# Kernel optimization log

Measured on AMD Instinct MI355X. Metric: run time of the kernel, lower is better.

Reference implementation:

```python
import jax, jax.numpy as jnp
import numpy as np

B, S, D, H = 2, 2048, 1024, 16
DEPTH = D // H


def setup_inputs() -> dict:
    key = jax.random.key(0)
    ks = jax.random.split(key, 8)
    w_scale = 0.02
    # causal mask: 1.0 where attention is NOT allowed (added as mask * -1e9)
    causal = jnp.triu(jnp.ones((S, S), dtype=jnp.float32), k=1)[None, None]  # [1,1,S,S]
    return {
        "q": jax.random.normal(ks[0], (B, S, D), dtype=jnp.float32),
        "k": jax.random.normal(ks[1], (B, S, D), dtype=jnp.float32),
        "v": jax.random.normal(ks[2], (B, S, D), dtype=jnp.float32),
        "mask": causal,
        "Wq": jax.random.normal(ks[3], (D, D), dtype=jnp.float32) * w_scale,
        "bq": jnp.zeros((D,), dtype=jnp.float32),
        "Wk": jax.random.normal(ks[4], (D, D), dtype=jnp.float32) * w_scale,
        "bk": jnp.zeros((D,), dtype=jnp.float32),
        "Wv": jax.random.normal(ks[5], (D, D), dtype=jnp.float32) * w_scale,
        "bv": jnp.zeros((D,), dtype=jnp.float32),
        "Wo": jax.random.normal(ks[6], (D, D), dtype=jnp.float32) * w_scale,
        "bo": jnp.zeros((D,), dtype=jnp.float32),
    }


def _split_heads(x):
    # [B,S,D] -> [B,H,S,depth]
    return x.reshape(B, S, H, DEPTH).transpose(0, 2, 1, 3)


def reference(q, k, v, mask, Wq, bq, Wk, bk, Wv, bv, Wo, bo):
    qh = _split_heads(q @ Wq + bq)
    kh = _split_heads(k @ Wk + bk)
    vh = _split_heads(v @ Wv + bv)
    scale = 1.0 / jnp.sqrt(jnp.asarray(DEPTH, dtype=qh.dtype))
    logits = jnp.einsum('bhqd,bhkd->bhqk', qh, kh) * scale  # [B,H,S,S]
    logits = logits + mask * (-1e9)
    attn = jax.nn.softmax(logits, axis=-1)
    out = jnp.einsum('bhqk,bhkd->bhqd', attn, vh)  # [B,H,S,depth]
    out = out.transpose(0, 2, 1, 3).reshape(B, S, D)
    return out @ Wo + bo
```

## Files before the change

kernel.cpp:

```cpp
#include <hip/hip_runtime.h>


typedef unsigned short u16;
typedef unsigned int u32;

using bf16x8 = __attribute__((ext_vector_type(8))) short;
using bf16x4 = __attribute__((ext_vector_type(4))) short;
using f32x4  = __attribute__((ext_vector_type(4))) float;

#define SEQ 2048
#define DMODEL 1024
#define NHEAD 16
#define DEPTH 64
#define BATCH 2
#define M_ROWS (BATCH * SEQ)

__device__ __forceinline__ u16 f2bf(float f) {
    union { float f; u32 u; } v; v.f = f;
    u32 u = v.u;
    return (u16)((u + 0x7FFFu + ((u >> 16) & 1u)) >> 16);
}
__device__ __forceinline__ u16 f2bf_trunc(float f) {
    union { float f; u32 u; } v; v.f = f;
    return (u16)(v.u >> 16);
}

__device__ __forceinline__ float hw_exp2(float x) {
#if __has_builtin(__builtin_amdgcn_exp2f)
    return __builtin_amdgcn_exp2f(x);
#else
    float r;
    asm("v_exp_f32 %0, %1" : "=v"(r) : "v"(x));
    return r;
#endif
}

__device__ __forceinline__ f32x4 mfma16(bf16x8 a, bf16x8 b, f32x4 c) {
    return __builtin_amdgcn_mfma_f32_16x16x32_bf16(a, b, c, 0, 0, 0);
}

__device__ __forceinline__ void glds16(const u16* src, u16* dst) {
    __builtin_amdgcn_global_load_lds((const __attribute__((address_space(1))) void*)src,
                                     (__attribute__((address_space(3))) void*)dst,
                                     16, 0, 0);
}

__device__ __forceinline__ bf16x8 fragld(const u16* base, int lr, int gc) {
    return *(const bf16x8*)(base + lr * 64 + (((gc ^ lr) & 7) << 3));
}
__device__ __forceinline__ bf16x8 fragld32(const u16* base, int lr, int gc) {
    return *(const bf16x8*)(base + lr * 32 + (((gc ^ lr) & 3) << 3));
}

__global__ __launch_bounds__(256) void prep_kernel(
        const float* __restrict__ q, const float* __restrict__ k,
        const float* __restrict__ v,
        u16* __restrict__ qo, u16* __restrict__ ko, u16* __restrict__ vo,
        const float* __restrict__ Wq, const float* __restrict__ Wk,
        const float* __restrict__ Wv, const float* __restrict__ Wo,
        u16* __restrict__ Wqt, u16* __restrict__ Wkt,
        u16* __restrict__ Wvt, u16* __restrict__ Wot) {
    int bid = blockIdx.x;
    if (bid < 12288) {
        const float* in; u16* out;
        int z = bid >> 12, bx = bid & 4095;
        if (z == 0)      { in = q; out = qo; }
        else if (z == 1) { in = k; out = ko; }
        else             { in = v; out = vo; }
        int idx = bx * 256 + threadIdx.x;
        float4 val = ((const float4*)in)[idx];
        ushort4 o;
        o.x = f2bf(val.x); o.y = f2bf(val.y); o.z = f2bf(val.z); o.w = f2bf(val.w);
        ((ushort4*)out)[idx] = o;
    } else {
        __shared__ float tile[32][33];
        int wid = bid - 12288;
        int z = wid >> 10, rem = wid & 1023;
        const float* W; u16* Wt;
        switch (z) {
            case 0: W = Wq; Wt = Wqt; break;
            case 1: W = Wk; Wt = Wkt; break;
            case 2: W = Wv; Wt = Wvt; break;
            default: W = Wo; Wt = Wot; break;
        }
        int k0 = (rem & 31) * 32, n0 = (rem >> 5) * 32;
        int tx = threadIdx.x & 31, ty = threadIdx.x >> 5;
#pragma unroll
        for (int i = 0; i < 4; ++i)
            tile[ty + 8 * i][tx] = W[(size_t)(k0 + ty + 8 * i) * DMODEL + n0 + tx];
        __syncthreads();
#pragma unroll
        for (int i = 0; i < 4; ++i)
            Wt[(size_t)(n0 + ty + 8 * i) * DMODEL + k0 + tx] = f2bf(tile[tx][ty + 8 * i]);
    }
}

template<int TM>
__device__ __forceinline__ void gemm_core(const u16* __restrict__ A, const u16* __restrict__ Bt,
                                          const float* __restrict__ bias,
                                          u16* __restrict__ outb, float* __restrict__ outf,
                                          int mode, float oscale, int bm0, int bn0) {
    constexpr int K = DMODEL;
    constexpr int NT = K / 32;
    constexpr int MI = TM / 32;
    constexpr int ACH = TM / 64;
    __shared__ u16 As[2][TM * 32];
    __shared__ u16 Bs[2][128 * 32];
    int t = threadIdx.x;
    int w = t >> 6, lane = t & 63, l15 = lane & 15, quad = lane >> 4;
    int wm = (w >> 1) * (TM / 2), wn = (w & 1) * 64;
    int r16 = lane >> 2, g4 = lane & 3;
    int gswz = ((g4 ^ (r16 & 3)) << 3);
    f32x4 acc[MI][4] = {};

#define QSTAGE(p, kt) do { \
    _Pragma("unroll") for (int c = 0; c < ACH; ++c) { \
        int ch = w * ACH + c; \
        glds16(A + (size_t)(bm0 + ch * 16 + r16) * K + (kt) * 32 + gswz, &As[p][ch * 512]); } \
    _Pragma("unroll") for (int c = 0; c < 2; ++c) { \
        int ch = w * 2 + c; \
        glds16(Bt + (size_t)(bn0 + ch * 16 + r16) * K + (kt) * 32 + gswz, &Bs[p][ch * 512]); } \
    } while (0)

    QSTAGE(0, 0);
    __syncthreads();

    for (int kt = 0; kt < NT; ++kt) {
        int cur = kt & 1;
        if (kt + 1 < NT) QSTAGE(cur ^ 1, kt + 1);
        bf16x8 af[MI], bfr[4];
#pragma unroll
        for (int i = 0; i < MI; ++i) af[i]  = fragld32(&As[cur][0], wm + i * 16 + l15, quad);
#pragma unroll
        for (int j = 0; j < 4;  ++j) bfr[j] = fragld32(&Bs[cur][0], wn + j * 16 + l15, quad);
#pragma unroll
        for (int i = 0; i < MI; ++i)
#pragma unroll
            for (int j = 0; j < 4; ++j)
                acc[i][j] = mfma16(af[i], bfr[j], acc[i][j]);
        __syncthreads();
    }
#undef QSTAGE

#pragma unroll
    for (int i = 0; i < MI; ++i) {
        int row_g0 = bm0 + wm + i * 16 + quad * 4;
#pragma unroll
        for (int j = 0; j < 4; ++j) {
            int col_g = bn0 + wn + j * 16 + l15;
            float bsv = bias[col_g];
#pragma unroll
            for (int r = 0; r < 4; ++r) {
                float v = (acc[i][j][r] + bsv) * oscale;
                int rg = row_g0 + r;
                if (mode == 2) {
                    outf[(size_t)rg * DMODEL + col_g] = v;
                } else {
                    int b = rg >> 11, s = rg & (SEQ - 1);
                    int h = col_g >> 6, d = col_g & 63;
                    size_t idx;
                    if (mode == 0) idx = ((size_t)(b * NHEAD + h) * SEQ + s) * DEPTH + d;
                    else           idx = ((size_t)(b * NHEAD + h) * DEPTH + d) * SEQ + s;
                    outb[idx] = f2bf(v);
                }
            }
        }
    }
}

#define SCALE_Q 0.1803368801111204f

__global__ __launch_bounds__(256, 4) void gemm_qkv(
        const u16* __restrict__ qb, const u16* __restrict__ kb, const u16* __restrict__ vb,
        const u16* __restrict__ Wqt, const u16* __restrict__ Wkt, const u16* __restrict__ Wvt,
        const float* __restrict__ bq, const float* __restrict__ bk, const float* __restrict__ bv,
        u16* __restrict__ Qp, u16* __restrict__ Kp, u16* __restrict__ Vpt) {
    int id = blockIdx.x;
    int c = id & 7, m = id >> 3;
    int slab = c * 12 + (m >> 3);
    int x = m & 7;
    int z = slab >> 5, y = slab & 31;
    int bm0 = y * 128, bn0 = x * 128;
    if (z == 0)      gemm_core<128>(qb, Wqt, bq, Qp,  nullptr, 0, SCALE_Q, bm0, bn0);
    else if (z == 1) gemm_core<128>(kb, Wkt, bk, Kp,  nullptr, 0, 1.0f,    bm0, bn0);
    else             gemm_core<128>(vb, Wvt, bv, Vpt, nullptr, 1, 1.0f,    bm0, bn0);
}

__global__ __launch_bounds__(256, 4) void gemm_out(
        const u16* __restrict__ attnb, const u16* __restrict__ Wot,
        const float* __restrict__ bo, float* __restrict__ out) {
    int id = blockIdx.x;
    int c = id & 7, m = id >> 3;
    int slab = c * 8 + (m >> 3);
    int x = m & 7;
    gemm_core<64>(attnb, Wot, bo, nullptr, out, 2, 1.0f, slab * 64, x * 128);
}

#define LP 72
__global__ __launch_bounds__(256) void attn_kernel(
        const u16* __restrict__ Qp, const u16* __restrict__ Kp,
        const u16* __restrict__ Vpt, u16* __restrict__ attn_out) {
    __shared__ u16 Klds[2][64 * 64];
    __shared__ u16 Vtlds[3][64 * 64];
    __shared__ u16 Plds[4 * 16 * LP];
    int t = threadIdx.x, w = t >> 6, lane = t & 63, l15 = lane & 15, quad = lane >> 4;
    int r8 = lane >> 3, g8 = lane & 7;
    int gswz = ((g8 ^ r8) << 3);
    u16* Pw = Plds + w * 16 * LP;

    int id = blockIdx.x;
    int xcd = id & 7, li = id >> 3;
    int bh = xcd * 4 + (li & 3);
    int pi = li >> 2;
    int b = bh >> 4, h = bh & 15;
    const u16* Qbase = Qp  + (size_t)bh * SEQ * DEPTH;
    const u16* Kbase = Kp  + (size_t)bh * SEQ * DEPTH;
    const u16* Vbase = Vpt + (size_t)bh * DEPTH * SEQ;

    bf16x8 ones;
#pragma unroll
    for (int i = 0; i < 8; ++i) ones[i] = (short)0x3F80;

    for (int half = 0; half < 2; ++half) {
        int qt = half ? pi : (31 - pi);
        int q0 = qt * 64;
        int nkt = qt + 1;
        __syncthreads();

        int qrow = q0 + w * 16 + l15;
        bf16x8 qf[2];
        qf[0] = *(const bf16x8*)(Qbase + (size_t)qrow * DEPTH + quad * 8);
        qf[1] = *(const bf16x8*)(Qbase + (size_t)qrow * DEPTH + 32 + quad * 8);

        f32x4 of[4] = {};
        f32x4 lacc = {};
        bf16x8 pfp[2];

#pragma unroll
        for (int c2 = 0; c2 < 2; ++c2) {
            int ch = w * 2 + c2;
            glds16(Kbase + (size_t)(ch * 8 + r8) * DEPTH + gswz, Klds[0] + ch * 512);
            glds16(Vbase + (size_t)(ch * 8 + r8) * SEQ + gswz,   Vtlds[0] + ch * 512);
        }

        for (int kt = 0; kt < nkt; ++kt) {
            int kc = kt & 1;
            __syncthreads();
            if (kt + 1 < nkt) {
                int kn = kt + 1, knx = kn & 1, vnx = kn % 3;
#pragma unroll
                for (int c2 = 0; c2 < 2; ++c2) {
                    int ch = w * 2 + c2;
                    glds16(Kbase + (size_t)(kn * 64 + ch * 8 + r8) * DEPTH + gswz,
                           Klds[knx] + ch * 512);
                    glds16(Vbase + (size_t)(ch * 8 + r8) * SEQ + kn * 64 + gswz,
                           Vtlds[vnx] + ch * 512);
                }
            }
            f32x4 st[4] = {};
            __builtin_amdgcn_s_setprio(1);
#pragma unroll
            for (int nt = 0; nt < 4; ++nt)
#pragma unroll
                for (int kk = 0; kk < 2; ++kk)
                    st[nt] = mfma16(fragld(Klds[kc], nt * 16 + l15, kk * 4 + quad), qf[kk], st[nt]);
            __builtin_amdgcn_s_setprio(0);

            if (kt > 0) {
                int vp = (kt - 1) % 3;
                __builtin_amdgcn_s_setprio(1);
#pragma unroll
                for (int kk = 0; kk < 2; ++kk) {
                    lacc = mfma16(pfp[kk], ones, lacc);
#pragma unroll
                    for (int nt = 0; nt < 4; ++nt)
                        of[nt] = mfma16(pfp[kk], fragld(Vtlds[vp], nt * 16 + l15, kk * 4 + quad), of[nt]);
                }
                __builtin_amdgcn_s_setprio(0);
            }

            bool diag = (kt == nkt - 1);
            int qlv = w * 16 + l15;
#pragma unroll
            for (int nt = 0; nt < 4; ++nt) {
                bf16x4 pv;
#pragma unroll
                for (int r = 0; r < 4; ++r) {
                    float e = hw_exp2(st[nt][r]);
                    if (diag) {
                        int keyl = nt * 16 + quad * 4 + r;
                        e = (keyl > qlv) ? 0.f : e;
                    }
                    pv[r] = (short)f2bf_trunc(e);
                }
                *(bf16x4*)(Pw + l15 * LP + nt * 16 + quad * 4) = pv;
            }
            asm volatile("" ::: "memory");
            pfp[0] = *(const bf16x8*)(Pw + l15 * LP + quad * 8);
            pfp[1] = *(const bf16x8*)(Pw + l15 * LP + 32 + quad * 8);
        }
        {
            int vp = (nkt - 1) % 3;
            __builtin_amdgcn_s_setprio(1);
#pragma unroll
            for (int kk = 0; kk < 2; ++kk) {
                lacc = mfma16(pfp[kk], ones, lacc);
#pragma unroll
                for (int nt = 0; nt < 4; ++nt)
                    of[nt] = mfma16(pfp[kk], fragld(Vtlds[vp], nt * 16 + l15, kk * 4 + quad), of[nt]);
            }
            __builtin_amdgcn_s_setprio(0);
        }
#pragma unroll
        for (int r = 0; r < 4; ++r) {
            float inv = 1.0f / lacc[r];
            int s_ = q0 + w * 16 + quad * 4 + r;
#pragma unroll
            for (int nt = 0; nt < 4; ++nt) {
                int dcol = h * DEPTH + nt * 16 + l15;
                attn_out[((size_t)(b * SEQ + s_)) * DMODEL + dcol] = f2bf(of[nt][r] * inv);
            }
        }
    }
}

extern "C" void kernel_launch(void* const* d_in, const int* in_sizes, int n_in,
                              void* d_out, int out_size, void* d_ws, size_t ws_size,
                              hipStream_t stream) {
    const float* q  = (const float*)d_in[0];
    const float* k  = (const float*)d_in[1];
    const float* v  = (const float*)d_in[2];
    const float* Wq = (const float*)d_in[4];
    const float* bq = (const float*)d_in[5];
    const float* Wk = (const float*)d_in[6];
    const float* bk = (const float*)d_in[7];
    const float* Wv = (const float*)d_in[8];
    const float* bv = (const float*)d_in[9];
    const float* Wo = (const float*)d_in[10];
    const float* bo = (const float*)d_in[11];
    float* out = (float*)d_out;

    char* ws = (char*)d_ws;
    const size_t SZ_ACT = (size_t)M_ROWS * DMODEL * 2;
    const size_t SZ_W   = (size_t)DMODEL * DMODEL * 2;
    u16* qb   = (u16*)(ws);
    u16* kb   = (u16*)(ws + SZ_ACT);
    u16* vb   = (u16*)(ws + 2 * SZ_ACT);
    u16* Wqt  = (u16*)(ws + 3 * SZ_ACT);
    u16* Wkt  = (u16*)(ws + 3 * SZ_ACT + SZ_W);
    u16* Wvt  = (u16*)(ws + 3 * SZ_ACT + 2 * SZ_W);
    u16* Wot  = (u16*)(ws + 3 * SZ_ACT + 3 * SZ_W);
    u16* Qp   = (u16*)(ws + 3 * SZ_ACT + 4 * SZ_W);
    u16* Kp   = (u16*)(ws + 4 * SZ_ACT + 4 * SZ_W);
    u16* Vpt  = (u16*)(ws + 5 * SZ_ACT + 4 * SZ_W);
    u16* attnb= (u16*)(ws + 6 * SZ_ACT + 4 * SZ_W);

    prep_kernel<<<dim3(16384), 256, 0, stream>>>(q, k, v, qb, kb, vb,
                                                 Wq, Wk, Wv, Wo, Wqt, Wkt, Wvt, Wot);
    gemm_qkv<<<dim3(768), 256, 0, stream>>>(
        qb, kb, vb, Wqt, Wkt, Wvt, bq, bk, bv, Qp, Kp, Vpt);
    attn_kernel<<<dim3(512), 256, 0, stream>>>(Qp, Kp, Vpt, attnb);
    gemm_out<<<dim3(512), 256, 0, stream>>>(attnb, Wot, bo, out);
}
```

Baseline: 219.0 us.

## Process two KV tiles per barrier with four-deep K/V LDS ring

The attention inner loop now handles key tiles in pairs, prefetching the next two K/V tiles into a 4-slot LDS ring, and issues one __syncthreads per pair instead of per tile. Both QK^T products are computed before the two softmax/PV steps, which replaces the earlier skewed software pipeline in which PV of the previous tile overlapped the current QK. The aim is fewer barriers and more independent MFMA work per sync. In exchange it uses more LDS (Klds grows from 2 to 4 slots, Vtlds from 3 to 4), which may reduce occupancy, and it adds register pressure from two sets of score accumulators.

```diff
diff --git a/kernel.cpp b/kernel.cpp
--- a/kernel.cpp
+++ b/kernel.cpp
@@ -200,8 +200,8 @@
 __global__ __launch_bounds__(256) void attn_kernel(
         const u16* __restrict__ Qp, const u16* __restrict__ Kp,
         const u16* __restrict__ Vpt, u16* __restrict__ attn_out) {
-    __shared__ u16 Klds[2][64 * 64];
-    __shared__ u16 Vtlds[3][64 * 64];
+    __shared__ u16 Klds[4][64 * 64];
+    __shared__ u16 Vtlds[4][64 * 64];
     __shared__ u16 Plds[4 * 16 * LP];
     int t = threadIdx.x, w = t >> 6, lane = t & 63, l15 = lane & 15, quad = lane >> 4;
     int r8 = lane >> 3, g8 = lane & 7;
@@ -221,6 +221,16 @@
 #pragma unroll
     for (int i = 0; i < 8; ++i) ones[i] = (short)0x3F80;
 
+#define STAGE_KV(ktv) do { \
+    int _b3 = (ktv) & 3; \
+    _Pragma("unroll") for (int c2 = 0; c2 < 2; ++c2) { \
+        int ch = w * 2 + c2; \
+        glds16(Kbase + (size_t)((ktv) * 64 + ch * 8 + r8) * DEPTH + gswz, \
+               Klds[_b3] + ch * 512); \
+        glds16(Vbase + (size_t)(ch * 8 + r8) * SEQ + (ktv) * 64 + gswz, \
+               Vtlds[_b3] + ch * 512); } \
+    } while (0)
+
     for (int half = 0; half < 2; ++half) {
         int qt = half ? pi : (31 - pi);
         int q0 = qt * 64;
@@ -234,51 +244,11 @@
 
         f32x4 of[4] = {};
         f32x4 lacc = {};
-        bf16x8 pfp[2];
-
-#pragma unroll
-        for (int c2 = 0; c2 < 2; ++c2) {
-            int ch = w * 2 + c2;
-            glds16(Kbase + (size_t)(ch * 8 + r8) * DEPTH + gswz, Klds[0] + ch * 512);
-            glds16(Vbase + (size_t)(ch * 8 + r8) * SEQ + gswz,   Vtlds[0] + ch * 512);
-        }
-
-        for (int kt = 0; kt < nkt; ++kt) {
-            int kc = kt & 1;
-            __syncthreads();
-            if (kt + 1 < nkt) {
-                int kn = kt + 1, knx = kn & 1, vnx = kn % 3;
-#pragma unroll
-                for (int c2 = 0; c2 < 2; ++c2) {
-                    int ch = w * 2 + c2;
-                    glds16(Kbase + (size_t)(kn * 64 + ch * 8 + r8) * DEPTH + gswz,
-                           Klds[knx] + ch * 512);
-                    glds16(Vbase + (size_t)(ch * 8 + r8) * SEQ + kn * 64 + gswz,
-                           Vtlds[vnx] + ch * 512);
-                }
-            }
-            f32x4 st[4] = {};
-            __builtin_amdgcn_s_setprio(1);
-#pragma unroll
-            for (int nt = 0; nt < 4; ++nt)
-#pragma unroll
-                for (int kk = 0; kk < 2; ++kk)
-                    st[nt] = mfma16(fragld(Klds[kc], nt * 16 + l15, kk * 4 + quad), qf[kk], st[nt]);
-            __builtin_amdgcn_s_setprio(0);
-
-            if (kt > 0) {
-                int vp = (kt - 1) % 3;
-                __builtin_amdgcn_s_setprio(1);
-#pragma unroll
-                for (int kk = 0; kk < 2; ++kk) {
-                    lacc = mfma16(pfp[kk], ones, lacc);
-#pragma unroll
-                    for (int nt = 0; nt < 4; ++nt)
-                        of[nt] = mfma16(pfp[kk], fragld(Vtlds[vp], nt * 16 + l15, kk * 4 + quad), of[nt]);
-                }
-                __builtin_amdgcn_s_setprio(0);
-            }
-
+
+        STAGE_KV(0);
+        if (nkt > 1) STAGE_KV(1);
+
+        auto smpv = [&](f32x4* st, int kt) {
             bool diag = (kt == nkt - 1);
             int qlv = w * 16 + l15;
 #pragma unroll
@@ -296,20 +266,51 @@
                 *(bf16x4*)(Pw + l15 * LP + nt * 16 + quad * 4) = pv;
             }
             asm volatile("" ::: "memory");
-            pfp[0] = *(const bf16x8*)(Pw + l15 * LP + quad * 8);
-            pfp[1] = *(const bf16x8*)(Pw + l15 * LP + 32 + quad * 8);
-        }
-        {
-            int vp = (nkt - 1) % 3;
+            bf16x8 pf[2];
+            pf[0] = *(const bf16x8*)(Pw + l15 * LP + quad * 8);
+            pf[1] = *(const bf16x8*)(Pw + l15 * LP + 32 + quad * 8);
+            asm volatile("" ::: "memory");
+            const u16* Vb = Vtlds[kt & 3];
             __builtin_amdgcn_s_setprio(1);
 #pragma unroll
             for (int kk = 0; kk < 2; ++kk) {
-                lacc = mfma16(pfp[kk], ones, lacc);
+                lacc = mfma16(pf[kk], ones, lacc);
 #pragma unroll
                 for (int nt = 0; nt < 4; ++nt)
-                    of[nt] = mfma16(pfp[kk], fragld(Vtlds[vp], nt * 16 + l15, kk * 4 + quad), of[nt]);
+                    of[nt] = mfma16(pf[kk], fragld(Vb, nt * 16 + l15, kk * 4 + quad), of[nt]);
             }
             __builtin_amdgcn_s_setprio(0);
+        };
+
+        for (int kt = 0; kt < nkt; kt += 2) {
+            __syncthreads();
+            bool pair = (kt + 1 < nkt);
+            if (kt + 2 < nkt) STAGE_KV(kt + 2);
+            if (kt + 3 < nkt) STAGE_KV(kt + 3);
+
+            f32x4 st0[4] = {}, st1[4] = {};
+            {
+                const u16* Kb = Klds[kt & 3];
+                __builtin_amdgcn_s_setprio(1);
+#pragma unroll
+                for (int nt = 0; nt < 4; ++nt)
+#pragma unroll
+                    for (int kk = 0; kk < 2; ++kk)
+                        st0[nt] = mfma16(fragld(Kb, nt * 16 + l15, kk * 4 + quad), qf[kk], st0[nt]);
+                __builtin_amdgcn_s_setprio(0);
+            }
+            if (pair) {
+                const u16* Kb = Klds[(kt + 1) & 3];
+                __builtin_amdgcn_s_setprio(1);
+#pragma unroll
+                for (int nt = 0; nt < 4; ++nt)
+#pragma unroll
+                    for (int kk = 0; kk < 2; ++kk)
+                        st1[nt] = mfma16(fragld(Kb, nt * 16 + l15, kk * 4 + quad), qf[kk], st1[nt]);
+                __builtin_amdgcn_s_setprio(0);
+            }
+            smpv(st0, kt);
+            if (pair) smpv(st1, kt + 1);
         }
 #pragma unroll
         for (int r = 0; r < 4; ++r) {
@@ -322,6 +323,7 @@
             }
         }
     }
+#undef STAGE_KV
 }
 
 extern "C" void kernel_launch(void* const* d_in, const int* in_sizes, int n_in,
```

Result: no change. 217.9 us (-0.5%).

## Load V fragments directly from global into registers instead of via LDS

Applied to the files above, without the earlier changes.

Drops the triple-buffered V tile in shared memory. Each wave now loads its V^T fragments straight from global memory into registers at the top of every key tile. The PV product is no longer deferred by one iteration; it runs in the same iteration right after P is computed. This removes LDS traffic and LDS footprint for V, which may improve occupancy, but adds redundant global loads across the four waves (each loads the full 64x64 V tile). It also loses the software pipelining that overlapped PV with the next QK^T.

```diff
diff --git a/kernel.cpp b/kernel.cpp
--- a/kernel.cpp
+++ b/kernel.cpp
@@ -201,7 +201,6 @@
         const u16* __restrict__ Qp, const u16* __restrict__ Kp,
         const u16* __restrict__ Vpt, u16* __restrict__ attn_out) {
     __shared__ u16 Klds[2][64 * 64];
-    __shared__ u16 Vtlds[3][64 * 64];
     __shared__ u16 Plds[4 * 16 * LP];
     int t = threadIdx.x, w = t >> 6, lane = t & 63, l15 = lane & 15, quad = lane >> 4;
     int r8 = lane >> 3, g8 = lane & 7;
@@ -234,27 +233,31 @@
 
         f32x4 of[4] = {};
         f32x4 lacc = {};
-        bf16x8 pfp[2];
 
 #pragma unroll
         for (int c2 = 0; c2 < 2; ++c2) {
             int ch = w * 2 + c2;
             glds16(Kbase + (size_t)(ch * 8 + r8) * DEPTH + gswz, Klds[0] + ch * 512);
-            glds16(Vbase + (size_t)(ch * 8 + r8) * SEQ + gswz,   Vtlds[0] + ch * 512);
         }
 
         for (int kt = 0; kt < nkt; ++kt) {
             int kc = kt & 1;
             __syncthreads();
+            bf16x8 vf[2][4];
+#pragma unroll
+            for (int kk = 0; kk < 2; ++kk)
+#pragma unroll
+                for (int nt = 0; nt < 4; ++nt)
+                    vf[kk][nt] = *(const bf16x8*)(Vbase + (size_t)(nt * 16 + l15) * SEQ
+                                                  + kt * 64 + (kk * 4 + quad) * 8);
+            asm volatile("" ::: "memory");
             if (kt + 1 < nkt) {
-                int kn = kt + 1, knx = kn & 1, vnx = kn % 3;
+                int nx = kc ^ 1, kn = kt + 1;
 #pragma unroll
                 for (int c2 = 0; c2 < 2; ++c2) {
                     int ch = w * 2 + c2;
                     glds16(Kbase + (size_t)(kn * 64 + ch * 8 + r8) * DEPTH + gswz,
-                           Klds[knx] + ch * 512);
-                    glds16(Vbase + (size_t)(ch * 8 + r8) * SEQ + kn * 64 + gswz,
-                           Vtlds[vnx] + ch * 512);
+                           Klds[nx] + ch * 512);
                 }
             }
             f32x4 st[4] = {};
@@ -265,19 +268,6 @@
                 for (int kk = 0; kk < 2; ++kk)
                     st[nt] = mfma16(fragld(Klds[kc], nt * 16 + l15, kk * 4 + quad), qf[kk], st[nt]);
             __builtin_amdgcn_s_setprio(0);
-
-            if (kt > 0) {
-                int vp = (kt - 1) % 3;
-                __builtin_amdgcn_s_setprio(1);
-#pragma unroll
-                for (int kk = 0; kk < 2; ++kk) {
-                    lacc = mfma16(pfp[kk], ones, lacc);
-#pragma unroll
-                    for (int nt = 0; nt < 4; ++nt)
-                        of[nt] = mfma16(pfp[kk], fragld(Vtlds[vp], nt * 16 + l15, kk * 4 + quad), of[nt]);
-                }
-                __builtin_amdgcn_s_setprio(0);
-            }
 
             bool diag = (kt == nkt - 1);
             int qlv = w * 16 + l15;
@@ -296,18 +286,16 @@
                 *(bf16x4*)(Pw + l15 * LP + nt * 16 + quad * 4) = pv;
             }
             asm volatile("" ::: "memory");
-            pfp[0] = *(const bf16x8*)(Pw + l15 * LP + quad * 8);
-            pfp[1] = *(const bf16x8*)(Pw + l15 * LP + 32 + quad * 8);
-        }
-        {
-            int vp = (nkt - 1) % 3;
+            bf16x8 pf[2];
+            pf[0] = *(const bf16x8*)(Pw + l15 * LP + quad * 8);
+            pf[1] = *(const bf16x8*)(Pw + l15 * LP + 32 + quad * 8);
             __builtin_amdgcn_s_setprio(1);
 #pragma unroll
             for (int kk = 0; kk < 2; ++kk) {
-                lacc = mfma16(pfp[kk], ones, lacc);
+                lacc = mfma16(pf[kk], ones, lacc);
 #pragma unroll
                 for (int nt = 0; nt < 4; ++nt)
-                    of[nt] = mfma16(pfp[kk], fragld(Vtlds[vp], nt * 16 + l15, kk * 4 + quad), of[nt]);
+                    of[nt] = mfma16(pf[kk], vf[kk][nt], of[nt]);
             }
             __builtin_amdgcn_s_setprio(0);
         }
```

Result: slower. 249.1 us (+13.8%).
